# Optimization experiments

Measured on AMD Instinct MI355X. Metric: run time of the kernel, lower is better.

Reference implementation:

```python
import jax, jax.numpy as jnp
import numpy as np

D_MODEL = 1024
NUM_HEADS = 16
D_HEAD = D_MODEL // NUM_HEADS
NEG_BIG = 10000000000.0  # matches the torch module's -1e10 mask constant


def setup_inputs() -> dict:
    key = jax.random.key(0)
    ks = jax.random.split(key, 9)
    d = D_MODEL
    scale = 1.0 / np.sqrt(d)
    inp = {
        "x": jax.random.normal(ks[0], (2, 2048, d), dtype=jnp.float32),
        "W_q": jax.random.normal(ks[1], (d, d), dtype=jnp.float32) * scale,
        "b_q": jnp.zeros((d,), dtype=jnp.float32),
        "W_k": jax.random.normal(ks[2], (d, d), dtype=jnp.float32) * scale,
        "b_k": jnp.zeros((d,), dtype=jnp.float32),
        "W_v": jax.random.normal(ks[3], (d, d), dtype=jnp.float32) * scale,
        "b_v": jnp.zeros((d,), dtype=jnp.float32),
        "W_o": jax.random.normal(ks[4], (d, d), dtype=jnp.float32) * scale,
        "b_o": jnp.zeros((d,), dtype=jnp.float32),
    }
    return inp


def reference(x, W_q, b_q, W_k, b_k, W_v, b_v, W_o, b_o):
    B, S, d = x.shape
    H, Dh = NUM_HEADS, D_HEAD

    Q = x @ W_q + b_q  # [B,S,d]
    K = x @ W_k + b_k
    V = x @ W_v + b_v

    # split heads: [B,S,d] -> [B,H,S,Dh]
    Qh = Q.reshape(B, S, H, Dh).transpose(0, 2, 1, 3)
    Kh = K.reshape(B, S, H, Dh).transpose(0, 2, 1, 3)
    Vh = V.reshape(B, S, H, Dh).transpose(0, 2, 1, 3)

    scores = jnp.einsum("bhid,bhjd->bhij", Qh, Kh) / jnp.sqrt(
        jnp.asarray(Dh, dtype=x.dtype)
    )

    # causal mask: tril(scores) - 1e10 * (1 - tril_mask)
    causal = jnp.tril(jnp.ones((S, S), dtype=x.dtype))
    scores = scores * causal - NEG_BIG * (1.0 - causal)

    attn = jax.nn.softmax(scores, axis=-1)  # dropout p=0.0 -> identity

    vals = jnp.einsum("bhij,bhjd->bhid", attn, Vh)  # [B,H,S,Dh]
    vals = vals.transpose(0, 2, 1, 3).reshape(B, S, d)

    return vals @ W_o + b_o
```

## Files before the change

kernel.cpp:

```cpp
#include <hip/hip_runtime.h>

typedef unsigned short u16;
typedef __attribute__((ext_vector_type(8))) short short8;
typedef __attribute__((ext_vector_type(4))) short shortx4;
typedef __attribute__((ext_vector_type(4))) float floatx4;

#define S_ 2048
#define D_ 1024
#define DQKV_ 3072
#define H_ 16
#define DH_ 64

#define EXP2F(x) __builtin_amdgcn_exp2f(x)

__device__ __forceinline__ float bf2f(u16 x) {
    union { unsigned int u; float f; } v; v.u = ((unsigned int)x) << 16; return v.f;
}
__device__ __forceinline__ u16 f2bf(float f) {
    unsigned int u = __float_as_uint(f);
    return (u16)((u + 0x7fffu + ((u >> 16) & 1u)) >> 16);
}
__device__ __forceinline__ u16 f2bf_fast(float f) {
    return (u16)((__float_as_uint(f) + 0x8000u) >> 16);
}

__device__ __forceinline__ void async16(const void* g, void* l) {
    __builtin_amdgcn_global_load_lds(
        (const __attribute__((address_space(1))) unsigned int*)g,
        (__attribute__((address_space(3))) unsigned int*)l, 16, 0, 0);
}

__global__ __launch_bounds__(256) void convert_x(const float* __restrict__ x, u16* __restrict__ xb) {
    const size_t i = ((size_t)blockIdx.x * 256 + threadIdx.x) * 4;
    float4 v = *(const float4*)&x[i];
    shortx4 h;
    h[0] = (short)f2bf(v.x); h[1] = (short)f2bf(v.y);
    h[2] = (short)f2bf(v.z); h[3] = (short)f2bf(v.w);
    *(shortx4*)&xb[i] = h;
}

__global__ __launch_bounds__(256) void transpose_w4(const float* __restrict__ Wq, const float* __restrict__ Wk,
                                                    const float* __restrict__ Wv, const float* __restrict__ Wo,
                                                    u16* __restrict__ Wqkvt, u16* __restrict__ Wot) {
    __shared__ u16 tile[32][33];
    const int z = blockIdx.z;
    const float* W = (z == 0) ? Wq : (z == 1) ? Wk : (z == 2) ? Wv : Wo;
    u16* dst = (z == 3) ? Wot : (Wqkvt + (size_t)z * D_ * D_);
    const int tx = threadIdx.x, ty = threadIdx.y;
    const int n0 = blockIdx.x * 32, k0 = blockIdx.y * 32;
#pragma unroll
    for (int r = 0; r < 4; ++r) {
        int k = ty + r * 8;
        tile[k][tx] = f2bf(W[(size_t)(k0 + k) * D_ + n0 + tx]);
    }
    __syncthreads();
#pragma unroll
    for (int r = 0; r < 4; ++r) {
        int n = ty + r * 8;
        dst[(size_t)(n0 + n) * D_ + k0 + tx] = tile[tx][n];
    }
}

__global__ __launch_bounds__(256) void transpose_headV(const u16* __restrict__ QKV, u16* __restrict__ Vt) {
    __shared__ u16 tile[64 * 65];
    const int t = threadIdx.x;
    const int bh = blockIdx.y, b = bh >> 4, h = bh & 15;
    const int s0 = blockIdx.x << 6;
#pragma unroll
    for (int i = 0; i < 16; ++i) {
        int idx = t + (i << 8);
        int s = idx >> 6, d = idx & 63;
        tile[s * 65 + d] = QKV[(size_t)(b * S_ + s0 + s) * DQKV_ + 2048 + h * DH_ + d];
    }
    __syncthreads();
#pragma unroll
    for (int i = 0; i < 16; ++i) {
        int idx = t + (i << 8);
        int d = idx >> 6, s = idx & 63;
        Vt[((size_t)bh * DH_ + d) * S_ + s0 + s] = tile[s * 65 + d];
    }
}

template <int BM, int BN, bool OUTF32>
__global__ __launch_bounds__(256) void gemm_bt(const u16* __restrict__ A, const u16* __restrict__ Bt,
                                               const float* __restrict__ b0, const float* __restrict__ b1,
                                               const float* __restrict__ b2, void* __restrict__ Cp,
                                               int M, int N, int Kd) {
    constexpr int FI = BM / 32, FJ = BN / 32;
    __shared__ __align__(16) u16 As[BM * 32];
    __shared__ __align__(16) u16 Bs[BN * 32];
    const int t = threadIdx.x;
    const int m0 = blockIdx.y * BM, n0 = blockIdx.x * BN;
    const int w = t >> 6, lane = t & 63;
    const int lr = lane & 15, lg = lane >> 4;
    const int wm = (w >> 1) * (BM / 2), wn = (w & 1) * (BN / 2);
    const int srow = lane >> 2, scol = (lane & 3) << 3;
    floatx4 acc[FI][FJ] = {};

    for (int k0 = 0; k0 < Kd; k0 += 32) {
#pragma unroll
        for (int c = 0; c < BM / 64; ++c) {
            int rbase = (w * (BM / 64) + c) * 16;
            async16(&A[(size_t)(m0 + rbase + srow) * Kd + k0 + scol], &As[rbase * 32]);
        }
#pragma unroll
        for (int c = 0; c < BN / 64; ++c) {
            int rbase = (w * (BN / 64) + c) * 16;
            async16(&Bt[(size_t)(n0 + rbase + srow) * Kd + k0 + scol], &Bs[rbase * 32]);
        }
        __syncthreads();
        short8 af[FI], bfr[FJ];
#pragma unroll
        for (int i = 0; i < FI; ++i) af[i]  = *(const short8*)&As[(wm + i * 16 + lr) * 32 + lg * 8];
#pragma unroll
        for (int j = 0; j < FJ; ++j) bfr[j] = *(const short8*)&Bs[(wn + j * 16 + lr) * 32 + lg * 8];
#pragma unroll
        for (int i = 0; i < FI; ++i)
#pragma unroll
            for (int j = 0; j < FJ; ++j)
                acc[i][j] = __builtin_amdgcn_mfma_f32_16x16x32_bf16(af[i], bfr[j], acc[i][j], 0, 0, 0);
        __syncthreads();
    }

#pragma unroll
    for (int j = 0; j < FJ; ++j) {
        int col = n0 + wn + j * 16 + lr;
        const float* bp = (col < 1024) ? b0 : (col < 2048) ? b1 : b2;
        float bv = bp[col & 1023];
#pragma unroll
        for (int i = 0; i < FI; ++i) {
            int rb = m0 + wm + i * 16 + lg * 4;
#pragma unroll
            for (int ii = 0; ii < 4; ++ii) {
                float val = acc[i][j][ii] + bv;
                if (OUTF32) ((float*)Cp)[(size_t)(rb + ii) * N + col] = val;
                else        ((u16*)Cp)[(size_t)(rb + ii) * N + col] = f2bf(val);
            }
        }
    }
}

__global__ __launch_bounds__(256) void attn_mfma(const u16* __restrict__ QKV, const u16* __restrict__ Vt,
                                                 u16* __restrict__ O) {
    __shared__ __align__(16) u16 Ks[64 * 72];
    __shared__ __align__(16) u16 Vs[64 * 72];
    __shared__ __align__(16) u16 Ps[4 * 16 * 76];
    const int t = threadIdx.x, w = t >> 6, lane = t & 63;
    const int lr = lane & 15, lg = lane >> 4;
    const int bh = blockIdx.x, b = bh >> 4, h = bh & 15;
    const int qt = 31 - blockIdx.y;
    const int q0 = qt << 6;
    const float cs = 0.18033688f;

    const u16* Kb  = QKV + (size_t)b * S_ * DQKV_ + 1024 + h * DH_;
    const u16* Vtb = Vt + (size_t)bh * DH_ * S_;
    u16* Pw = Ps + w * (16 * 76);

    short8 qf[2];
#pragma unroll
    for (int ks = 0; ks < 2; ++ks)
        qf[ks] = *(const short8*)&QKV[(size_t)(b * S_ + q0 + w * 16 + lr) * DQKV_ + h * DH_ + ks * 32 + lg * 8];

    floatx4 of[4] = {};
    float lsum[4] = {0.f, 0.f, 0.f, 0.f};

    for (int kb = 0; kb <= qt; ++kb) {
        const int K0 = kb << 6;
#pragma unroll
        for (int c = 0; c < 2; ++c) {
            int idx = t + (c << 8);
            int row = idx >> 3, c8 = (idx & 7) << 3;
            *(uint4*)&Ks[row * 72 + c8] = *(const uint4*)&Kb[(size_t)(K0 + row) * DQKV_ + c8];
            *(uint4*)&Vs[row * 72 + c8] = *(const uint4*)&Vtb[(size_t)row * S_ + K0 + c8];
        }
        __syncthreads();

        floatx4 sf[4] = {};
#pragma unroll
        for (int ks = 0; ks < 2; ++ks)
#pragma unroll
            for (int j = 0; j < 4; ++j) {
                short8 kf = *(const short8*)&Ks[(j * 16 + lr) * 72 + ks * 32 + lg * 8];
                sf[j] = __builtin_amdgcn_mfma_f32_16x16x32_bf16(qf[ks], kf, sf[j], 0, 0, 0);
            }

        const bool diag = (kb == qt);
#pragma unroll
        for (int j = 0; j < 4; ++j)
#pragma unroll
            for (int ii = 0; ii < 4; ++ii) {
                float ev = EXP2F(sf[j][ii] * cs);
                if (diag && (j * 16 + lr > w * 16 + lg * 4 + ii)) ev = 0.f;
                lsum[ii] += ev;
                Pw[(lg * 4 + ii) * 76 + j * 16 + lr] = f2bf_fast(ev);
            }

#pragma unroll
        for (int ks = 0; ks < 2; ++ks) {
            union { short8 v; shortx4 hh[2]; } pa;
            pa.hh[0] = *(const shortx4*)&Pw[lr * 76 + ks * 32 + lg * 8];
            pa.hh[1] = *(const shortx4*)&Pw[lr * 76 + ks * 32 + lg * 8 + 4];
#pragma unroll
            for (int j = 0; j < 4; ++j) {
                short8 vf = *(const short8*)&Vs[(j * 16 + lr) * 72 + ks * 32 + lg * 8];
                of[j] = __builtin_amdgcn_mfma_f32_16x16x32_bf16(pa.v, vf, of[j], 0, 0, 0);
            }
        }
        __syncthreads();
    }

    float rinv[4];
#pragma unroll
    for (int ii = 0; ii < 4; ++ii) {
        float s = lsum[ii];
#pragma unroll
        for (int off = 1; off < 16; off <<= 1) s += __shfl_xor(s, off);
        rinv[ii] = 1.f / s;
    }
#pragma unroll
    for (int j = 0; j < 4; ++j)
#pragma unroll
        for (int ii = 0; ii < 4; ++ii)
            O[(size_t)(b * S_ + q0 + w * 16 + lg * 4 + ii) * D_ + h * DH_ + j * 16 + lr] =
                f2bf(of[j][ii] * rinv[ii]);
}

extern "C" void kernel_launch(void* const* d_in, const int* in_sizes, int n_in,
                              void* d_out, int out_size, void* d_ws, size_t ws_size,
                              hipStream_t stream) {
    (void)in_sizes; (void)n_in; (void)out_size; (void)ws_size;
    const float* x  = (const float*)d_in[0];
    const float* Wq = (const float*)d_in[1];
    const float* bq = (const float*)d_in[2];
    const float* Wk = (const float*)d_in[3];
    const float* bk = (const float*)d_in[4];
    const float* Wv = (const float*)d_in[5];
    const float* bv = (const float*)d_in[6];
    const float* Wo = (const float*)d_in[7];
    const float* bo = (const float*)d_in[8];

    u16* ws    = (u16*)d_ws;
    u16* WqkvT = ws;
    u16* WoT   = ws + (size_t)3 * (1 << 20);
    u16* QKV   = ws + (size_t)4 * (1 << 20);
    u16* Vtm   = ws + (size_t)16 * (1 << 20);
    u16* xbf   = ws + (size_t)20 * (1 << 20);
    u16* Am    = ws + (size_t)20 * (1 << 20);

    convert_x<<<4096, 256, 0, stream>>>(x, xbf);
    transpose_w4<<<dim3(32, 32, 4), dim3(32, 8), 0, stream>>>(Wq, Wk, Wv, Wo, WqkvT, WoT);

    gemm_bt<128, 128, false><<<dim3(DQKV_ / 128, 4096 / 128), 256, 0, stream>>>(
        xbf, WqkvT, bq, bk, bv, QKV, 4096, DQKV_, 1024);

    transpose_headV<<<dim3(32, 32), 256, 0, stream>>>(QKV, Vtm);

    attn_mfma<<<dim3(32, 32), 256, 0, stream>>>(QKV, Vtm, Am);

    gemm_bt<64, 128, true><<<dim3(1024 / 128, 4096 / 64), 256, 0, stream>>>(
        Am, WoT, bo, bo, bo, d_out, 4096, 1024, 1024);
}
```

Before: 212.1 us.

## Double-buffer K/V tiles with async LDS loads and XOR swizzle in attention

The attention kernel now keeps two LDS buffers for the K and V tiles. The next tile is prefetched with async global-to-LDS copies while the current tile is being computed, and the trailing barrier in each iteration is dropped. The padded 72-element row stride is replaced by a 64-element stride with an XOR swizzle on 16-byte chunks, to avoid bank conflicts while matching the async copy layout. This doubles K/V shared memory and depends on the async copies being complete before the barrier.

```diff
diff --git a/kernel.cpp b/kernel.cpp
--- a/kernel.cpp
+++ b/kernel.cpp
@@ -142,8 +142,8 @@
 
 __global__ __launch_bounds__(256) void attn_mfma(const u16* __restrict__ QKV, const u16* __restrict__ Vt,
                                                  u16* __restrict__ O) {
-    __shared__ __align__(16) u16 Ks[64 * 72];
-    __shared__ __align__(16) u16 Vs[64 * 72];
+    __shared__ __align__(16) u16 KsA[2][64 * 64];
+    __shared__ __align__(16) u16 VsA[2][64 * 64];
     __shared__ __align__(16) u16 Ps[4 * 16 * 76];
     const int t = threadIdx.x, w = t >> 6, lane = t & 63;
     const int lr = lane & 15, lg = lane >> 4;
@@ -156,6 +156,10 @@
     const u16* Vtb = Vt + (size_t)bh * DH_ * S_;
     u16* Pw = Ps + w * (16 * 76);
 
+    const int rb = lane >> 3;
+    const int cc = ((lane & 7) ^ rb) << 3;
+    const int swz = lr & 7;
+
     short8 qf[2];
 #pragma unroll
     for (int ks = 0; ks < 2; ++ks)
@@ -164,23 +168,36 @@
     floatx4 of[4] = {};
     float lsum[4] = {0.f, 0.f, 0.f, 0.f};
 
+    {
+        u16* Kd = &KsA[0][w * 512];
+        u16* Vd = &VsA[0][w * 512];
+        async16(&Kb[(size_t)(w * 8 + rb) * DQKV_ + cc], Kd);
+        async16(&Kb[(size_t)(32 + w * 8 + rb) * DQKV_ + cc], Kd + 2048);
+        async16(&Vtb[(size_t)(w * 8 + rb) * S_ + cc], Vd);
+        async16(&Vtb[(size_t)(32 + w * 8 + rb) * S_ + cc], Vd + 2048);
+    }
+
     for (int kb = 0; kb <= qt; ++kb) {
-        const int K0 = kb << 6;
-#pragma unroll
-        for (int c = 0; c < 2; ++c) {
-            int idx = t + (c << 8);
-            int row = idx >> 3, c8 = (idx & 7) << 3;
-            *(uint4*)&Ks[row * 72 + c8] = *(const uint4*)&Kb[(size_t)(K0 + row) * DQKV_ + c8];
-            *(uint4*)&Vs[row * 72 + c8] = *(const uint4*)&Vtb[(size_t)row * S_ + K0 + c8];
-        }
+        const int cur = kb & 1;
         __syncthreads();
+        if (kb < qt) {
+            const int K1 = (kb + 1) << 6;
+            u16* Kd = &KsA[cur ^ 1][w * 512];
+            u16* Vd = &VsA[cur ^ 1][w * 512];
+            async16(&Kb[(size_t)(K1 + w * 8 + rb) * DQKV_ + cc], Kd);
+            async16(&Kb[(size_t)(K1 + 32 + w * 8 + rb) * DQKV_ + cc], Kd + 2048);
+            async16(&Vtb[(size_t)(w * 8 + rb) * S_ + K1 + cc], Vd);
+            async16(&Vtb[(size_t)(32 + w * 8 + rb) * S_ + K1 + cc], Vd + 2048);
+        }
+        const u16* Kc = KsA[cur];
+        const u16* Vc = VsA[cur];
 
         floatx4 sf[4] = {};
 #pragma unroll
         for (int ks = 0; ks < 2; ++ks)
 #pragma unroll
             for (int j = 0; j < 4; ++j) {
-                short8 kf = *(const short8*)&Ks[(j * 16 + lr) * 72 + ks * 32 + lg * 8];
+                short8 kf = *(const short8*)&Kc[(j * 16 + lr) * 64 + ((((ks << 2) + lg) ^ swz) << 3)];
                 sf[j] = __builtin_amdgcn_mfma_f32_16x16x32_bf16(qf[ks], kf, sf[j], 0, 0, 0);
             }
 
@@ -202,11 +219,10 @@
             pa.hh[1] = *(const shortx4*)&Pw[lr * 76 + ks * 32 + lg * 8 + 4];
 #pragma unroll
             for (int j = 0; j < 4; ++j) {
-                short8 vf = *(const short8*)&Vs[(j * 16 + lr) * 72 + ks * 32 + lg * 8];
+                short8 vf = *(const short8*)&Vc[(j * 16 + lr) * 64 + ((((ks << 2) + lg) ^ swz) << 3)];
                 of[j] = __builtin_amdgcn_mfma_f32_16x16x32_bf16(pa.v, vf, of[j], 0, 0, 0);
             }
         }
-        __syncthreads();
     }
 
     float rinv[4];
```

After: 194.5 us. 8.3% less time.
